# Kernel optimization log

Hardware: AMD Instinct MI355X
Metric: run time of the kernel (lower is better)

Reference implementation:

```python
import jax, jax.numpy as jnp
import numpy as np

B, S, D = 4, 2048, 1024
H, HD = 16, 64  # num_heads, head_size
NEG = -1e20


def setup_inputs() -> dict:
    key = jax.random.key(0)
    ks = jax.random.split(key, 8)
    query = jax.random.normal(ks[0], (B, S, D), dtype=jnp.float32)
    k_in = jax.random.normal(ks[1], (B, S, D), dtype=jnp.float32)
    v_in = jax.random.normal(ks[2], (B, S, D), dtype=jnp.float32)
    # causal mask: True where attention is DISALLOWED (masked_fill semantics)
    mask = jnp.triu(jnp.ones((S, S), dtype=bool), k=1)
    scale = 1.0 / np.sqrt(D)
    Wq = jax.random.normal(ks[3], (D, H * HD), dtype=jnp.float32) * scale
    Wk = jax.random.normal(ks[4], (D, H * HD), dtype=jnp.float32) * scale
    Wv = jax.random.normal(ks[5], (D, H * HD), dtype=jnp.float32) * scale
    Wo = jax.random.normal(ks[6], (H * HD, D), dtype=jnp.float32) * scale
    bo = jnp.zeros((D,), dtype=jnp.float32)
    return {"query": query, "key": k_in, "value": v_in, "mask": mask,
            "Wq": Wq, "Wk": Wk, "Wv": Wv, "Wo": Wo, "bo": bo}


def reference(query, key, value, mask, Wq, Wk, Wv, Wo, bo):
    # projections -> [B, H, S, HD]
    q = (query @ Wq).reshape(B, -1, H, HD).transpose(0, 2, 1, 3)
    k = (key @ Wk).reshape(B, -1, H, HD).transpose(0, 2, 1, 3)
    v = (value @ Wv).reshape(B, -1, H, HD).transpose(0, 2, 1, 3)
    # scaled dot-product attention with boolean mask (True = masked out)
    scores = jnp.einsum('bhqd,bhkd->bhqk', q, k) / jnp.sqrt(jnp.float32(HD))
    scores = jnp.where(mask, jnp.float32(NEG), scores)
    attn = jax.nn.softmax(scores, axis=-1)
    out = jnp.einsum('bhqk,bhkd->bhqd', attn, v)  # [B,H,S,HD]
    out = out.transpose(0, 2, 1, 3).reshape(B, -1, H * HD)
    return out @ Wo + bo
```

## Files before the change

kernel.cpp:

```cpp
#include <hip/hip_runtime.h>

#define B_ 4
#define S_ 2048
#define D_ 1024
#define H_ 16
#define HD_ 64

typedef __attribute__((ext_vector_type(8))) short bf16x8;
typedef __attribute__((ext_vector_type(4))) float f32x4;
typedef __attribute__((ext_vector_type(4))) unsigned u32x4;

__device__ __forceinline__ short f2bf(float f) {
  unsigned u = __builtin_bit_cast(unsigned, f);
  u += 0x7fffu + ((u >> 16) & 1u);
  return (short)(u >> 16);
}

__device__ __forceinline__ unsigned cvtpk(float a, float b) {
  unsigned r;
  asm("v_cvt_pk_bf16_f32 %0, %1, %2" : "=v"(r) : "v"(a), "v"(b));
  return r;
}

__device__ __forceinline__ void gload_lds16(const void* g, void* l) {
  __builtin_amdgcn_global_load_lds((const __attribute__((address_space(1))) void*)g,
                                   (__attribute__((address_space(3))) void*)l, 16, 0, 0);
}

__device__ __forceinline__ bf16x8 ldsw8(const short* base, int row, int colb) {
  const int off = (row * 128 + colb) ^ ((row & 7) << 4);
  return *(const bf16x8*)((const char*)base + off);
}

__device__ __forceinline__ int bpr_off(int row, int cbyte) {
  return ((row >> 1) << 7) + ((((row & 1) << 6) + cbyte) ^ (((row >> 1) & 7) << 4));
}

#define MFMA16(a, b, c) __builtin_amdgcn_mfma_f32_16x16x32_bf16((a), (b), (c), 0, 0, 0)

__global__ void transpose_cast_w4(const float* __restrict__ W0, const float* __restrict__ W1,
                                  const float* __restrict__ W2, const float* __restrict__ W3,
                                  short* __restrict__ T0, short* __restrict__ T1,
                                  short* __restrict__ T2, short* __restrict__ T3) {
  __shared__ float tile[32][33];
  const int z = blockIdx.z;
  const float* W = z == 0 ? W0 : z == 1 ? W1 : z == 2 ? W2 : W3;
  short* Wt = z == 0 ? T0 : z == 1 ? T1 : z == 2 ? T2 : T3;
  const int n0 = blockIdx.x * 32, k0 = blockIdx.y * 32;
  const int tx = threadIdx.x, ty = threadIdx.y;
  #pragma unroll
  for (int i = ty; i < 32; i += 8)
    tile[i][tx] = W[(size_t)(k0 + i) * 1024 + n0 + tx];
  __syncthreads();
  #pragma unroll
  for (int i = ty; i < 32; i += 8)
    Wt[(size_t)(n0 + i) * 1024 + k0 + tx] = f2bf(tile[tx][i]);
}

__global__ __launch_bounds__(256) void gemm_qkv(const float* __restrict__ Aq,
                                                const float* __restrict__ Ak,
                                                const float* __restrict__ Av,
                                                const short* __restrict__ Bq,
                                                const short* __restrict__ Bk,
                                                const short* __restrict__ Bv,
                                                short* __restrict__ Oq,
                                                short* __restrict__ Ok,
                                                short* __restrict__ Ov,
                                                float qscale) {
  __shared__ __align__(16) float Asf[2][128 * 32];
  __shared__ __align__(16) short Bs[2][128 * 32];
  const int z = blockIdx.z;
  const float* A = z == 0 ? Aq : z == 1 ? Ak : Av;
  const short* Bt = z == 0 ? Bq : z == 1 ? Bk : Bv;
  short* outb = z == 0 ? Oq : z == 1 ? Ok : Ov;
  const float oscale = z == 0 ? qscale : 1.0f;

  const int tid = threadIdx.x;
  const int l = tid & 63, w = tid >> 6;
  const int wm = w >> 1, wn = w & 1;
  const int flat = blockIdx.x + (blockIdx.y << 3);
  const int xcd = flat & 7, t = flat >> 3;
  const int row0 = (xcd * 8 + (t & 7)) * 128;
  const int col0 = (t >> 3) * 128;
  const int l15 = l & 15, lq = l >> 4;

  f32x4 acc[4][4] = {};

  auto stageA = [&](int k0, int buf) {
    #pragma unroll
    for (int i = 0; i < 4; i++) {
      const int eoff = w * 4096 + i * 1024 + l * 16;
      const int row = eoff >> 7;
      const int sc = (eoff & 127) ^ ((row & 7) << 4);
      gload_lds16((const char*)A + (size_t)(row0 + row) * 4096 + (size_t)k0 * 4 + sc,
                  (char*)Asf[buf] + w * 4096 + i * 1024);
    }
  };
  auto stageB = [&](int k0, int buf) {
    #pragma unroll
    for (int i = 0; i < 2; i++) {
      const int o = w * 2048 + i * 1024 + l * 16;
      const int row2 = o >> 7;
      const int ip = (o & 127) ^ ((row2 & 7) << 4);
      const int row = row2 * 2 + (ip >> 6);
      const int cb = ip & 63;
      gload_lds16((const char*)Bt + ((size_t)(col0 + row) * 1024 + k0) * 2 + cb,
                  (char*)Bs[buf] + o);
    }
  };

  stageA(0, 0);
  stageB(0, 0);

  for (int kt = 0; kt < 32; ++kt) {
    __syncthreads();
    if (kt + 1 < 32) {
      stageA((kt + 1) * 32, (kt + 1) & 1);
      stageB((kt + 1) * 32, (kt + 1) & 1);
    }
    const float* as = Asf[kt & 1];
    const short* bs = Bs[kt & 1];
    bf16x8 af[4], bfv[4];
    #pragma unroll
    for (int mf = 0; mf < 4; mf++) {
      const int R = wm * 64 + mf * 16 + l15;
      const int sw = (R & 7) << 4;
      const f32x4 g0 = *(const f32x4*)((const char*)as + R * 128 + ((lq * 32) ^ sw));
      const f32x4 g1 = *(const f32x4*)((const char*)as + R * 128 + ((lq * 32 + 16) ^ sw));
      const u32x4 uu = {cvtpk(g0[0], g0[1]), cvtpk(g0[2], g0[3]),
                        cvtpk(g1[0], g1[1]), cvtpk(g1[2], g1[3])};
      af[mf] = __builtin_bit_cast(bf16x8, uu);
    }
    #pragma unroll
    for (int nf = 0; nf < 4; nf++)
      bfv[nf] = *(const bf16x8*)((const char*)bs + bpr_off(wn * 64 + nf * 16 + l15, lq * 16));
    #pragma unroll
    for (int mf = 0; mf < 4; mf++)
      #pragma unroll
      for (int nf = 0; nf < 4; nf++)
        acc[mf][nf] = MFMA16(af[mf], bfv[nf], acc[mf][nf]);
  }

  #pragma unroll
  for (int mf = 0; mf < 4; mf++) {
    #pragma unroll
    for (int nf = 0; nf < 4; nf++) {
      #pragma unroll
      for (int r = 0; r < 4; r++) {
        const int gr = row0 + wm * 64 + mf * 16 + lq * 4 + r;
        const int gc = col0 + wn * 64 + nf * 16 + l15;
        const int b = gr >> 11, s = gr & 2047;
        const int h = gc >> 6, hd = gc & 63;
        const float v = acc[mf][nf][r];
        if (z < 2)
          outb[(((size_t)(b * H_ + h)) * S_ + s) * HD_ + hd] = f2bf(v * oscale);
        else
          outb[(((size_t)(b * H_ + h)) * HD_ + hd) * S_ + s] = f2bf(v);
      }
    }
  }
}

__global__ __launch_bounds__(256) void gemm_o(const short* __restrict__ A,
                                              const short* __restrict__ Bt,
                                              float* __restrict__ outf,
                                              const float* __restrict__ bias) {
  __shared__ __align__(16) short As[2][128 * 32];
  __shared__ __align__(16) short Bs[2][128 * 32];
  const int tid = threadIdx.x;
  const int l = tid & 63;
  const int w = tid >> 6;
  const int wm = w >> 1, wn = w & 1;
  const int flat = blockIdx.x + (blockIdx.y << 3);
  const int xcd = flat & 7, t = flat >> 3;
  const int row0 = (xcd * 8 + (t & 7)) * 128;
  const int col0 = (t >> 3) * 128;
  const int l15 = l & 15, lq = l >> 4;

  f32x4 acc[4][4] = {};

  auto stage = [&](const short* src, int r0, int k0, short* lds) {
    #pragma unroll
    for (int i = 0; i < 2; i++) {
      const int o = w * 2048 + i * 1024 + l * 16;
      const int row2 = o >> 7;
      const int ip = (o & 127) ^ ((row2 & 7) << 4);
      const int row = row2 * 2 + (ip >> 6);
      const int cb = ip & 63;
      gload_lds16((const char*)src + ((size_t)(r0 + row) * 1024 + k0) * 2 + cb,
                  (char*)lds + o);
    }
  };

  stage(A, row0, 0, As[0]);
  stage(Bt, col0, 0, Bs[0]);

  for (int kt = 0; kt < 32; ++kt) {
    __syncthreads();
    if (kt + 1 < 32) {
      stage(A, row0, (kt + 1) * 32, As[(kt + 1) & 1]);
      stage(Bt, col0, (kt + 1) * 32, Bs[(kt + 1) & 1]);
    }
    const short* as = As[kt & 1];
    const short* bs = Bs[kt & 1];
    bf16x8 af[4], bfv[4];
    #pragma unroll
    for (int mf = 0; mf < 4; mf++)
      af[mf] = *(const bf16x8*)((const char*)as + bpr_off(wm * 64 + mf * 16 + l15, lq * 16));
    #pragma unroll
    for (int nf = 0; nf < 4; nf++)
      bfv[nf] = *(const bf16x8*)((const char*)bs + bpr_off(wn * 64 + nf * 16 + l15, lq * 16));
    #pragma unroll
    for (int mf = 0; mf < 4; mf++)
      #pragma unroll
      for (int nf = 0; nf < 4; nf++)
        acc[mf][nf] = MFMA16(af[mf], bfv[nf], acc[mf][nf]);
  }

  #pragma unroll
  for (int mf = 0; mf < 4; mf++)
    #pragma unroll
    for (int nf = 0; nf < 4; nf++)
      #pragma unroll
      for (int r = 0; r < 4; r++) {
        const int gr = row0 + wm * 64 + mf * 16 + lq * 4 + r;
        const int gc = col0 + wn * 64 + nf * 16 + l15;
        outf[(size_t)gr * 1024 + gc] = acc[mf][nf][r] + bias[gc];
      }
}

__global__ __launch_bounds__(256) void attn_kernel(const short* __restrict__ Qh,
                                                   const short* __restrict__ Kh,
                                                   const short* __restrict__ Vtr,
                                                   short* __restrict__ attnout) {
  __shared__ __align__(16) short Ks[2][64 * 64];
  __shared__ __align__(16) short Vs[2][64 * 64];
  __shared__ __align__(16) short Ps[4][32 * 64];
  const int tid = threadIdx.x, l = tid & 63, w = tid >> 6;
  const int l15 = l & 15, lq = l >> 4;
  const int flat = blockIdx.x;
  const int vid = (flat & 7) * 64 + (flat >> 3);
  const int bh = vid >> 3, pairx = vid & 7;
  const int b = bh >> 4, h = bh & 15;
  const size_t base = (size_t)bh * (S_ * HD_);
  const short* Qp = Qh + base;
  const short* Kp = Kh + base;
  const short* Vp = Vtr + base;
  short* Pw = (short*)Ps[w];

  for (int pass = 0; pass < 2; ++pass) {
    const int qt = pass ? 15 - pairx : pairx;
    const int q0 = qt * 128;
    const int qw = q0 + w * 32;
    const int nkt = (q0 >> 6) + 2;

    bf16x8 qf[2][2];
    #pragma unroll
    for (int qh = 0; qh < 2; qh++)
      #pragma unroll
      for (int ks = 0; ks < 2; ks++)
        qf[qh][ks] = *(const bf16x8*)(Qp + (size_t)(qw + qh * 16 + l15) * 64 + ks * 32 + lq * 8);

    f32x4 oacc[4][2] = {};
    float mrow[2] = {-1e30f, -1e30f};
    float lpart[2] = {0.f, 0.f};

    auto stage = [&](int kt, int bf) {
      const int k0s = kt << 6;
      #pragma unroll
      for (int i = 0; i < 2; i++) {
        const int o = w * 2048 + i * 1024 + l * 16;
        const int sw = o ^ (((o >> 7) & 7) << 4);
        gload_lds16((const char*)Kp + (size_t)k0s * 128 + sw, (char*)Ks[bf] + o);
        gload_lds16(Vp + (size_t)(o >> 7) * S_ + k0s + ((sw & 127) >> 1), (char*)Vs[bf] + o);
      }
    };

    stage(0, 0);
    __syncthreads();

    for (int kt = 0; kt < nkt; ++kt) {
      const int cur = kt & 1;
      if (kt + 1 < nkt) stage(kt + 1, cur ^ 1);
      const int k0 = kt << 6;

      if (k0 <= qw + 31) {
        f32x4 sacc[2][4] = {};
        __builtin_amdgcn_s_setprio(1);
        #pragma unroll
        for (int ks = 0; ks < 2; ks++) {
          #pragma unroll
          for (int mf = 0; mf < 4; mf++) {
            const bf16x8 kf = ldsw8(Ks[cur], mf * 16 + l15, ks * 64 + lq * 16);
            #pragma unroll
            for (int qh = 0; qh < 2; qh++)
              sacc[qh][mf] = MFMA16(kf, qf[qh][ks], sacc[qh][mf]);
          }
        }
        __builtin_amdgcn_s_setprio(0);

        if (k0 + 63 > qw) {
          #pragma unroll
          for (int qh = 0; qh < 2; qh++) {
            const int qg = qw + qh * 16 + l15 - lq * 4;
            #pragma unroll
            for (int mf = 0; mf < 4; mf++)
              #pragma unroll
              for (int r = 0; r < 4; r++)
                if (k0 + mf * 16 + r > qg) sacc[qh][mf][r] = -1e30f;
          }
        }

        float mxl[2];
        #pragma unroll
        for (int qh = 0; qh < 2; qh++) {
          float t0 = fmaxf(fmaxf(sacc[qh][0][0], sacc[qh][0][1]),
                           fmaxf(sacc[qh][0][2], sacc[qh][0][3]));
          float t1 = fmaxf(fmaxf(sacc[qh][1][0], sacc[qh][1][1]),
                           fmaxf(sacc[qh][1][2], sacc[qh][1][3]));
          float t2 = fmaxf(fmaxf(sacc[qh][2][0], sacc[qh][2][1]),
                           fmaxf(sacc[qh][2][2], sacc[qh][2][3]));
          float t3 = fmaxf(fmaxf(sacc[qh][3][0], sacc[qh][3][1]),
                           fmaxf(sacc[qh][3][2], sacc[qh][3][3]));
          mxl[qh] = fmaxf(fmaxf(t0, t1), fmaxf(t2, t3));
        }

        const bool need = (mxl[0] > mrow[0] + 8.f) || (mxl[1] > mrow[1] + 8.f);
        if (__any(need)) {
          #pragma unroll
          for (int qh = 0; qh < 2; qh++) {
            float m = fmaxf(mxl[qh], __shfl_xor(mxl[qh], 16));
            m = fmaxf(m, __shfl_xor(m, 32));
            const float mn = fmaxf(mrow[qh], m);
            const float fac = __builtin_amdgcn_exp2f(mrow[qh] - mn);
            mrow[qh] = mn;
            lpart[qh] *= fac;
            #pragma unroll
            for (int mf = 0; mf < 4; mf++) oacc[mf][qh] *= fac;
          }
        }

        #pragma unroll
        for (int qh = 0; qh < 2; qh++) {
          float rs = 0.f;
          const int row = qh * 16 + l15;
          #pragma unroll
          for (int mf = 0; mf < 4; mf++) {
            f32x4 p;
            #pragma unroll
            for (int r = 0; r < 4; r++) {
              const float e = __builtin_amdgcn_exp2f(sacc[qh][mf][r] - mrow[qh]);
              p[r] = e;
              rs += e;
            }
            const int off = (row * 128 + mf * 32 + lq * 8) ^ ((row & 7) << 4);
            *(uint2*)((char*)Pw + off) = make_uint2(cvtpk(p[0], p[1]), cvtpk(p[2], p[3]));
          }
          lpart[qh] += rs;
        }

        asm volatile("s_waitcnt lgkmcnt(0)" ::: "memory");
        __builtin_amdgcn_sched_barrier(0);

        __builtin_amdgcn_s_setprio(1);
        #pragma unroll
        for (int ks = 0; ks < 2; ks++) {
          bf16x8 pb[2];
          #pragma unroll
          for (int qh = 0; qh < 2; qh++) {
            const int row = qh * 16 + l15;
            const int off = (row * 128 + ks * 64 + lq * 16) ^ ((row & 7) << 4);
            pb[qh] = *(const bf16x8*)((const char*)Pw + off);
          }
          #pragma unroll
          for (int mf = 0; mf < 4; mf++) {
            const bf16x8 vf = ldsw8(Vs[cur], mf * 16 + l15, ks * 64 + lq * 16);
            #pragma unroll
            for (int qh = 0; qh < 2; qh++)
              oacc[mf][qh] = MFMA16(vf, pb[qh], oacc[mf][qh]);
          }
        }
        __builtin_amdgcn_s_setprio(0);
      }
      __syncthreads();
    }

    #pragma unroll
    for (int qh = 0; qh < 2; qh++) {
      float lr = lpart[qh];
      lr += __shfl_xor(lr, 16);
      lr += __shfl_xor(lr, 32);
      const float rinv = __builtin_amdgcn_rcpf(lr);
      const int q = qw + qh * 16 + l15;
      #pragma unroll
      for (int mf = 0; mf < 4; mf++) {
        const f32x4 o = oacc[mf][qh];
        const uint2 u = make_uint2(cvtpk(o[0] * rinv, o[1] * rinv),
                                   cvtpk(o[2] * rinv, o[3] * rinv));
        *(uint2*)(attnout + ((size_t)b * S_ + q) * (H_ * HD_) + h * 64 + mf * 16 + lq * 4) = u;
      }
    }
  }
}

extern "C" void kernel_launch(void* const* d_in, const int* in_sizes, int n_in,
                              void* d_out, int out_size, void* d_ws, size_t ws_size,
                              hipStream_t stream) {
  const float* query = (const float*)d_in[0];
  const float* key_  = (const float*)d_in[1];
  const float* value = (const float*)d_in[2];
  const float* Wq = (const float*)d_in[4];
  const float* Wk = (const float*)d_in[5];
  const float* Wv = (const float*)d_in[6];
  const float* Wo = (const float*)d_in[7];
  const float* bo = (const float*)d_in[8];
  float* out = (float*)d_out;

  char* ws = (char*)d_ws;
  const size_t MB = (size_t)1 << 20;
  short* Xbuf = (short*)(ws);
  short* Wqt  = (short*)(ws + 16 * MB);
  short* Wkt  = (short*)(ws + 18 * MB);
  short* Wvt  = (short*)(ws + 20 * MB);
  short* Wot  = (short*)(ws + 22 * MB);
  short* Qh   = (short*)(ws + 24 * MB);
  short* Kh   = (short*)(ws + 40 * MB);
  short* Vt   = (short*)(ws + 56 * MB);

  const dim3 tb(32, 8);
  const dim3 tg4(32, 32, 4);
  const float QSCALE = 0.125f * 1.4426950408889634f;

  transpose_cast_w4<<<tg4, tb, 0, stream>>>(Wq, Wk, Wv, Wo, Wqt, Wkt, Wvt, Wot);

  gemm_qkv<<<dim3(8, 64, 3), 256, 0, stream>>>(query, key_, value, Wqt, Wkt, Wvt,
                                               Qh, Kh, Vt, QSCALE);

  attn_kernel<<<dim3(512), 256, 0, stream>>>(Qh, Kh, Vt, Xbuf);

  gemm_o<<<dim3(8, 64), 256, 0, stream>>>(Xbuf, Wot, out, bo);
}
```

Before: 198.6 us.

## Convert QKV GEMM A tiles to bf16 via registers before LDS store

The QKV projection GEMM previously copied fp32 A tiles directly into LDS and converted them to bf16 on each fragment read. It now loads A into registers, converts each element to bf16 once after the MFMAs, and writes it to a bf16 LDS buffer using the same layout as B. This halves A's LDS footprint and read traffic and removes redundant conversions. The cost is extra VGPRs for the in-flight A data and a register-staged load path that no longer uses direct global-to-LDS copies.

```diff
diff --git a/kernel.cpp b/kernel.cpp
--- a/kernel.cpp
+++ b/kernel.cpp
@@ -67,7 +67,7 @@
                                                 short* __restrict__ Ok,
                                                 short* __restrict__ Ov,
                                                 float qscale) {
-  __shared__ __align__(16) float Asf[2][128 * 32];
+  __shared__ __align__(16) short Asb[2][128 * 32];
   __shared__ __align__(16) short Bs[2][128 * 32];
   const int z = blockIdx.z;
   const float* A = z == 0 ? Aq : z == 1 ? Ak : Av;
@@ -86,15 +86,20 @@
 
   f32x4 acc[4][4] = {};
 
-  auto stageA = [&](int k0, int buf) {
-    #pragma unroll
-    for (int i = 0; i < 4; i++) {
-      const int eoff = w * 4096 + i * 1024 + l * 16;
-      const int row = eoff >> 7;
-      const int sc = (eoff & 127) ^ ((row & 7) << 4);
-      gload_lds16((const char*)A + (size_t)(row0 + row) * 4096 + (size_t)k0 * 4 + sc,
-                  (char*)Asf[buf] + w * 4096 + i * 1024);
-    }
+  const int ar = tid >> 1, ac = (tid & 1) * 16;
+  const float* Ap = A + (size_t)(row0 + ar) * 1024 + ac;
+  float4 ra0, ra1, ra2, ra3;
+  auto loadA = [&](int kt) {
+    const float4* p = (const float4*)(Ap + kt * 32);
+    ra0 = p[0]; ra1 = p[1]; ra2 = p[2]; ra3 = p[3];
+  };
+  auto writeA = [&](int buf) {
+    const u32x4 w0 = {cvtpk(ra0.x, ra0.y), cvtpk(ra0.z, ra0.w),
+                      cvtpk(ra1.x, ra1.y), cvtpk(ra1.z, ra1.w)};
+    const u32x4 w1 = {cvtpk(ra2.x, ra2.y), cvtpk(ra2.z, ra2.w),
+                      cvtpk(ra3.x, ra3.y), cvtpk(ra3.z, ra3.w)};
+    *(u32x4*)((char*)Asb[buf] + bpr_off(ar, ac * 2)) = w0;
+    *(u32x4*)((char*)Asb[buf] + bpr_off(ar, ac * 2 + 16)) = w1;
   };
   auto stageB = [&](int k0, int buf) {
     #pragma unroll
@@ -109,28 +114,22 @@
     }
   };
 
-  stageA(0, 0);
+  loadA(0);
   stageB(0, 0);
+  writeA(0);
 
   for (int kt = 0; kt < 32; ++kt) {
     __syncthreads();
     if (kt + 1 < 32) {
-      stageA((kt + 1) * 32, (kt + 1) & 1);
+      loadA(kt + 1);
       stageB((kt + 1) * 32, (kt + 1) & 1);
     }
-    const float* as = Asf[kt & 1];
+    const short* as = Asb[kt & 1];
     const short* bs = Bs[kt & 1];
     bf16x8 af[4], bfv[4];
     #pragma unroll
-    for (int mf = 0; mf < 4; mf++) {
-      const int R = wm * 64 + mf * 16 + l15;
-      const int sw = (R & 7) << 4;
-      const f32x4 g0 = *(const f32x4*)((const char*)as + R * 128 + ((lq * 32) ^ sw));
-      const f32x4 g1 = *(const f32x4*)((const char*)as + R * 128 + ((lq * 32 + 16) ^ sw));
-      const u32x4 uu = {cvtpk(g0[0], g0[1]), cvtpk(g0[2], g0[3]),
-                        cvtpk(g1[0], g1[1]), cvtpk(g1[2], g1[3])};
-      af[mf] = __builtin_bit_cast(bf16x8, uu);
-    }
+    for (int mf = 0; mf < 4; mf++)
+      af[mf] = *(const bf16x8*)((const char*)as + bpr_off(wm * 64 + mf * 16 + l15, lq * 16));
     #pragma unroll
     for (int nf = 0; nf < 4; nf++)
       bfv[nf] = *(const bf16x8*)((const char*)bs + bpr_off(wn * 64 + nf * 16 + l15, lq * 16));
@@ -139,6 +138,7 @@
       #pragma unroll
       for (int nf = 0; nf < 4; nf++)
         acc[mf][nf] = MFMA16(af[mf], bfv[nf], acc[mf][nf]);
+    if (kt + 1 < 32) writeA((kt + 1) & 1);
   }
 
   #pragma unroll
```

Measured after the change: 202.9 us. +2.2%, slower.
